# Optimization experiments

Hardware: AMD Instinct MI355X
Metric: run time of the kernel (lower is better)

## Reference

```python
import jax, jax.numpy as jnp
import numpy as np
from jax import lax

B, S, C = 32, 4096, 512   # batch, seq_len, input_dim
P, K = 3, 10              # pairs_per_fan_in, max_fan_in


def setup_inputs() -> dict:
    key = jax.random.key(0)
    keys = jax.random.split(key, K + 1)
    inp = {"x": jax.random.normal(keys[0], (B, S, C), dtype=jnp.float32)}
    for k in range(1, K + 1):
        # WIO layout: (kernel_width=k, in_channels=C, out_channels=P)
        fan_in = C * k
        scale = 1.0 / np.sqrt(fan_in)  # kaiming-uniform-ish scale
        inp[f"w{k}"] = scale * jax.random.normal(keys[k], (k, C, P), dtype=jnp.float32)
    return inp


def _causal_conv(x, w):
    # x: (B, S, C), w: (k, C, P) -> (B, S, P); left-pad k-1 == torch padding=k-1 then [:, :, :S]
    k = w.shape[0]
    return lax.conv_general_dilated(
        x, w, window_strides=(1,), padding=[(k - 1, 0)],
        dimension_numbers=("NWC", "WIO", "NWC"))


def reference(x, w1, w2, w3, w4, w5, w6, w7, w8, w9, w10) -> jnp.ndarray:
    ws = (w1, w2, w3, w4, w5, w6, w7, w8, w9, w10)
    # ReLU each causal conv output, concat along feature dim -> (B, S, K*P)
    parts = [jax.nn.relu(_causal_conv(x, w)) for w in ws]
    return jnp.concatenate(parts, axis=-1)
```

## Files before the change

### kernel.cpp

```cpp
#include <hip/hip_runtime.h>

typedef __attribute__((ext_vector_type(8))) short short8;
typedef __attribute__((ext_vector_type(4))) short short4v;
typedef __attribute__((ext_vector_type(4))) float f32x4;

#define C_DIM 512
#define S_DIM 4096
#define NCOL 165
#define NCOLP 176
#define LDK 40
#define M_TILE 80
#define M_OUT 64
#define BK 32
#define NCHUNK 16

__device__ __forceinline__ unsigned short f2bf(float f) {
  unsigned u = __builtin_bit_cast(unsigned, f);
  u += 0x7fffu + ((u >> 16) & 1u);
  return (unsigned short)(u >> 16);
}
__device__ __forceinline__ float bf2f(unsigned short h) {
  unsigned u = ((unsigned)h) << 16;
  return __builtin_bit_cast(float, u);
}

struct WP { const float* w[10]; };

__global__ __launch_bounds__(256) void prep_kernel(WP wp, unsigned short* bt_hi,
                                                   unsigned short* bt_lo) {
  int idx = blockIdx.x * 256 + threadIdx.x;
  int col = idx >> 9;
  int c = idx & 511;
  float v = 0.f;
  if (col < NCOL) {
    int kw = 1, base = 0;
    while (col >= base + 3 * kw) { base += 3 * kw; ++kw; }
    int rem = col - base;
    int t = rem / 3, p = rem - 3 * t;
    v = wp.w[kw - 1][(t * C_DIM + c) * 3 + p];
  }
  unsigned short hi = f2bf(v);
  unsigned short lo = f2bf(v - bf2f(hi));
  bt_hi[col * C_DIM + c] = hi;
  bt_lo[col * C_DIM + c] = lo;
}

__global__ __launch_bounds__(256, 3) void conv_kernel(const float* __restrict__ x,
                                                      const unsigned short* __restrict__ bt_hi,
                                                      const unsigned short* __restrict__ bt_lo,
                                                      float* __restrict__ out) {
  __shared__ __align__(16) unsigned char smem[40960];
  unsigned short* As_hi = (unsigned short*)smem;
  unsigned short* As_lo = (unsigned short*)(smem + 6400);
  unsigned short* Bs_hi = (unsigned short*)(smem + 12800);
  unsigned short* Bs_lo = (unsigned short*)(smem + 26880);
  float* Ys = (float*)smem;

  const int tid = threadIdx.x;
  const int b = blockIdx.x >> 6;
  const int tile = blockIdx.x & 63;
  const int s0 = tile * M_OUT;
  const int sBase = s0 - 16;
  const int wave = tid >> 6;
  const int lane = tid & 63;
  const int lane15 = lane & 15;
  const int quad = lane >> 4;
  const int n0 = wave * 3;
  const int nmine = (wave < 3) ? 3 : 2;

  f32x4 acc[5][3];
#pragma unroll
  for (int m = 0; m < 5; ++m)
#pragma unroll
    for (int n = 0; n < 3; ++n) acc[m][n] = (f32x4){0.f, 0.f, 0.f, 0.f};

  for (int ch = 0; ch < NCHUNK; ++ch) {
    const int kc = ch * BK;
    for (int idx = tid; idx < 640; idx += 256) {
      int row = idx >> 3;
      int q = idx & 7;
      int s = sBase + row;
      float4 v = make_float4(0.f, 0.f, 0.f, 0.f);
      if (s >= 0) v = *(const float4*)&x[((size_t)(b * S_DIM + s)) * C_DIM + kc + q * 4];
      unsigned short h0 = f2bf(v.x), h1 = f2bf(v.y), h2 = f2bf(v.z), h3 = f2bf(v.w);
      unsigned short l0 = f2bf(v.x - bf2f(h0)), l1 = f2bf(v.y - bf2f(h1));
      unsigned short l2 = f2bf(v.z - bf2f(h2)), l3 = f2bf(v.w - bf2f(h3));
      short4v hv = {(short)h0, (short)h1, (short)h2, (short)h3};
      short4v lv = {(short)l0, (short)l1, (short)l2, (short)l3};
      *(short4v*)&As_hi[row * LDK + q * 4] = hv;
      *(short4v*)&As_lo[row * LDK + q * 4] = lv;
    }
    for (int idx = tid; idx < 1408; idx += 256) {
      int buf = (idx >= 704) ? 1 : 0;
      int rem = idx - buf * 704;
      int col = rem >> 2;
      int q = rem & 3;
      const unsigned short* src = buf ? bt_lo : bt_hi;
      unsigned short* dst = buf ? Bs_lo : Bs_hi;
      short8 v = *(const short8*)&src[col * C_DIM + kc + q * 8];
      *(short8*)&dst[col * LDK + q * 8] = v;
    }
    __syncthreads();
    short8 bh[3], bl[3];
#pragma unroll
    for (int nn = 0; nn < 3; ++nn) {
      if (nn < nmine) {
        int cr = (n0 + nn) * 16 + lane15;
        bh[nn] = *(const short8*)&Bs_hi[cr * LDK + quad * 8];
        bl[nn] = *(const short8*)&Bs_lo[cr * LDK + quad * 8];
      }
    }
#pragma unroll
    for (int m = 0; m < 5; ++m) {
      int ar = m * 16 + lane15;
      short8 ah = *(const short8*)&As_hi[ar * LDK + quad * 8];
      short8 al = *(const short8*)&As_lo[ar * LDK + quad * 8];
#pragma unroll
      for (int nn = 0; nn < 3; ++nn) {
        if (nn < nmine) {
          acc[m][nn] = __builtin_amdgcn_mfma_f32_16x16x32_bf16(ah, bh[nn], acc[m][nn], 0, 0, 0);
          acc[m][nn] = __builtin_amdgcn_mfma_f32_16x16x32_bf16(ah, bl[nn], acc[m][nn], 0, 0, 0);
          acc[m][nn] = __builtin_amdgcn_mfma_f32_16x16x32_bf16(al, bh[nn], acc[m][nn], 0, 0, 0);
        }
      }
    }
    __syncthreads();
  }

#pragma unroll
  for (int i = 1; i <= 4; ++i) {
    if (i == 1) {
#pragma unroll
      for (int nn = 0; nn < 3; ++nn)
        if (nn < nmine)
#pragma unroll
          for (int r = 0; r < 4; ++r)
            Ys[0 * 2816 + (quad * 4 + r) * NCOLP + (n0 + nn) * 16 + lane15] = acc[0][nn][r];
    }
#pragma unroll
    for (int nn = 0; nn < 3; ++nn)
      if (nn < nmine)
#pragma unroll
        for (int r = 0; r < 4; ++r)
          Ys[(i & 1) * 2816 + (quad * 4 + r) * NCOLP + (n0 + nn) * 16 + lane15] = acc[i][nn][r];
    __syncthreads();
    for (int o = tid; o < 480; o += 256) {
      int r = o / 30;
      int j = o - 30 * r;
      int kw = j / 3 + 1;
      int p = j - (kw - 1) * 3;
      int base = 3 * (kw * (kw - 1)) / 2;
      float sum = 0.f;
      for (int d = 0; d < kw; ++d) {
        int rr = r - d;
        int slot = (rr >= 0) ? (i & 1) : ((i ^ 1) & 1);
        int lr = (rr >= 0) ? rr : (16 + rr);
        int colv = base + (kw - 1 - d) * 3 + p;
        sum += Ys[slot * 2816 + lr * NCOLP + colv];
      }
      int s = s0 + 16 * (i - 1) + r;
      out[((size_t)(b * S_DIM + s)) * 30 + j] = fmaxf(sum, 0.f);
    }
    __syncthreads();
  }
}

extern "C" void kernel_launch(void* const* d_in, const int* in_sizes, int n_in,
                              void* d_out, int out_size, void* d_ws, size_t ws_size,
                              hipStream_t stream) {
  const float* x = (const float*)d_in[0];
  WP wp;
  for (int k = 0; k < 10; ++k) wp.w[k] = (const float*)d_in[k + 1];
  unsigned short* bt_hi = (unsigned short*)d_ws;
  unsigned short* bt_lo = bt_hi + NCOLP * C_DIM;
  prep_kernel<<<NCOLP * C_DIM / 256, 256, 0, stream>>>(wp, bt_hi, bt_lo);
  conv_kernel<<<32 * (S_DIM / M_OUT), 256, 0, stream>>>(x, bt_hi, bt_lo, (float*)d_out);
}
```

Before: 472.4 us.

## Prefetch A into registers, DMA B via global_load_lds, shrink LDS pitch

Loads of the next x chunk are issued into registers before the MFMA loop so global latency overlaps compute. The weight tiles are copied straight to LDS with global_load_lds 16-byte transfers instead of passing through registers. The bf16 hi/lo split is done with perm-packing, and the LDS row pitch drops from 40 to 32, which shrinks shared memory so occupancy can rise to 4 blocks per CU. The unpadded pitch may cause LDS bank conflicts on the MFMA fragment reads, and the extra prefetch registers could pressure the tighter launch bound.

```diff
diff --git a/kernel.cpp b/kernel.cpp
--- a/kernel.cpp
+++ b/kernel.cpp
@@ -1,14 +1,13 @@
 #include <hip/hip_runtime.h>
 
 typedef __attribute__((ext_vector_type(8))) short short8;
-typedef __attribute__((ext_vector_type(4))) short short4v;
 typedef __attribute__((ext_vector_type(4))) float f32x4;
 
 #define C_DIM 512
 #define S_DIM 4096
 #define NCOL 165
 #define NCOLP 176
-#define LDK 40
+#define LDK 32
 #define M_TILE 80
 #define M_OUT 64
 #define BK 32
@@ -45,15 +44,44 @@
   bt_lo[col * C_DIM + c] = lo;
 }
 
-__global__ __launch_bounds__(256, 3) void conv_kernel(const float* __restrict__ x,
+__device__ __forceinline__ void gld16(const void* g, void* l) {
+  __builtin_amdgcn_global_load_lds(
+      (const __attribute__((address_space(1))) unsigned int*)(const unsigned int*)g,
+      (__attribute__((address_space(3))) unsigned int*)(unsigned int*)l, 16, 0, 0);
+}
+
+__device__ __forceinline__ void cvt_pack(const float4 v, uint2& hi, uint2& lo) {
+  unsigned u0 = __builtin_bit_cast(unsigned, v.x);
+  unsigned u1 = __builtin_bit_cast(unsigned, v.y);
+  unsigned u2 = __builtin_bit_cast(unsigned, v.z);
+  unsigned u3 = __builtin_bit_cast(unsigned, v.w);
+  unsigned r0 = u0 + 0x7fffu + ((u0 >> 16) & 1u);
+  unsigned r1 = u1 + 0x7fffu + ((u1 >> 16) & 1u);
+  unsigned r2 = u2 + 0x7fffu + ((u2 >> 16) & 1u);
+  unsigned r3 = u3 + 0x7fffu + ((u3 >> 16) & 1u);
+  hi.x = __builtin_amdgcn_perm(r1, r0, 0x07060302u);
+  hi.y = __builtin_amdgcn_perm(r3, r2, 0x07060302u);
+  float m0 = v.x - __builtin_bit_cast(float, r0 & 0xffff0000u);
+  float m1 = v.y - __builtin_bit_cast(float, r1 & 0xffff0000u);
+  float m2 = v.z - __builtin_bit_cast(float, r2 & 0xffff0000u);
+  float m3 = v.w - __builtin_bit_cast(float, r3 & 0xffff0000u);
+  unsigned w0 = __builtin_bit_cast(unsigned, m0); w0 += 0x7fffu + ((w0 >> 16) & 1u);
+  unsigned w1 = __builtin_bit_cast(unsigned, m1); w1 += 0x7fffu + ((w1 >> 16) & 1u);
+  unsigned w2 = __builtin_bit_cast(unsigned, m2); w2 += 0x7fffu + ((w2 >> 16) & 1u);
+  unsigned w3 = __builtin_bit_cast(unsigned, m3); w3 += 0x7fffu + ((w3 >> 16) & 1u);
+  lo.x = __builtin_amdgcn_perm(w1, w0, 0x07060302u);
+  lo.y = __builtin_amdgcn_perm(w3, w2, 0x07060302u);
+}
+
+__global__ __launch_bounds__(256, 4) void conv_kernel(const float* __restrict__ x,
                                                       const unsigned short* __restrict__ bt_hi,
                                                       const unsigned short* __restrict__ bt_lo,
                                                       float* __restrict__ out) {
-  __shared__ __align__(16) unsigned char smem[40960];
+  __shared__ __align__(16) unsigned char smem[32768];
   unsigned short* As_hi = (unsigned short*)smem;
-  unsigned short* As_lo = (unsigned short*)(smem + 6400);
-  unsigned short* Bs_hi = (unsigned short*)(smem + 12800);
-  unsigned short* Bs_lo = (unsigned short*)(smem + 26880);
+  unsigned short* As_lo = (unsigned short*)(smem + 5120);
+  unsigned short* Bs_hi = (unsigned short*)(smem + 10240);
+  unsigned short* Bs_lo = (unsigned short*)(smem + 21504);
   float* Ys = (float*)smem;
 
   const int tid = threadIdx.x;
@@ -68,39 +96,65 @@
   const int n0 = wave * 3;
   const int nmine = (wave < 3) ? 3 : 2;
 
+  const float4* aptr[3];
+  bool aexists[3], avalid[3];
+  int arow[3], aq[3];
+#pragma unroll
+  for (int i = 0; i < 3; ++i) {
+    int idx = tid + i * 256;
+    aexists[i] = (idx < 640);
+    arow[i] = idx >> 3;
+    aq[i] = idx & 7;
+    int s = sBase + arow[i];
+    avalid[i] = aexists[i] && (s >= 0);
+    aptr[i] = (const float4*)&x[((size_t)(b * S_DIM + (s < 0 ? 0 : s))) * C_DIM + aq[i] * 4];
+  }
+
+  float4 pf[3];
   f32x4 acc[5][3];
 #pragma unroll
   for (int m = 0; m < 5; ++m)
 #pragma unroll
     for (int n = 0; n < 3; ++n) acc[m][n] = (f32x4){0.f, 0.f, 0.f, 0.f};
 
+  auto loadA = [&](int ch) {
+#pragma unroll
+    for (int i = 0; i < 3; ++i) {
+      if (avalid[i]) pf[i] = aptr[i][ch * 8];
+      else pf[i] = make_float4(0.f, 0.f, 0.f, 0.f);
+    }
+  };
+  auto cvtWrite = [&]() {
+#pragma unroll
+    for (int i = 0; i < 3; ++i) {
+      if (aexists[i]) {
+        uint2 hi, lo;
+        cvt_pack(pf[i], hi, lo);
+        *(uint2*)&As_hi[arow[i] * LDK + aq[i] * 4] = hi;
+        *(uint2*)&As_lo[arow[i] * LDK + aq[i] * 4] = lo;
+      }
+    }
+  };
+  auto dmaB = [&](int ch) {
+    const int kc = ch * BK;
+    for (int j = wave; j < 22; j += 4) {
+      int jj = (j < 11) ? j : j - 11;
+      const unsigned short* src = (j < 11) ? bt_hi : bt_lo;
+      unsigned short* dst = (j < 11) ? Bs_hi : Bs_lo;
+      int col = jj * 16 + (lane >> 2);
+      int part = lane & 3;
+      gld16(src + col * C_DIM + kc + part * 8, dst + jj * 512);
+    }
+  };
+
+  loadA(0);
+  cvtWrite();
+  dmaB(0);
+  __syncthreads();
+
   for (int ch = 0; ch < NCHUNK; ++ch) {
-    const int kc = ch * BK;
-    for (int idx = tid; idx < 640; idx += 256) {
-      int row = idx >> 3;
-      int q = idx & 7;
-      int s = sBase + row;
-      float4 v = make_float4(0.f, 0.f, 0.f, 0.f);
-      if (s >= 0) v = *(const float4*)&x[((size_t)(b * S_DIM + s)) * C_DIM + kc + q * 4];
-      unsigned short h0 = f2bf(v.x), h1 = f2bf(v.y), h2 = f2bf(v.z), h3 = f2bf(v.w);
-      unsigned short l0 = f2bf(v.x - bf2f(h0)), l1 = f2bf(v.y - bf2f(h1));
-      unsigned short l2 = f2bf(v.z - bf2f(h2)), l3 = f2bf(v.w - bf2f(h3));
-      short4v hv = {(short)h0, (short)h1, (short)h2, (short)h3};
-      short4v lv = {(short)l0, (short)l1, (short)l2, (short)l3};
-      *(short4v*)&As_hi[row * LDK + q * 4] = hv;
-      *(short4v*)&As_lo[row * LDK + q * 4] = lv;
-    }
-    for (int idx = tid; idx < 1408; idx += 256) {
-      int buf = (idx >= 704) ? 1 : 0;
-      int rem = idx - buf * 704;
-      int col = rem >> 2;
-      int q = rem & 3;
-      const unsigned short* src = buf ? bt_lo : bt_hi;
-      unsigned short* dst = buf ? Bs_lo : Bs_hi;
-      short8 v = *(const short8*)&src[col * C_DIM + kc + q * 8];
-      *(short8*)&dst[col * LDK + q * 8] = v;
-    }
-    __syncthreads();
+    if (ch < NCHUNK - 1) loadA(ch + 1);
+
     short8 bh[3], bl[3];
 #pragma unroll
     for (int nn = 0; nn < 3; ++nn) {
@@ -125,6 +179,11 @@
       }
     }
     __syncthreads();
+    if (ch < NCHUNK - 1) {
+      cvtWrite();
+      dmaB(ch + 1);
+      __syncthreads();
+    }
   }
 
 #pragma unroll
```

Measured after the change: 412.8 us. 12.6% less time.
